# Kernel optimization log

Hardware: AMD Instinct MI355X
Metric: run time of the kernel (lower is better)

Reference implementation:

```python
import jax, jax.numpy as jnp
import numpy as np

H = 16  # num_heads

def setup_inputs() -> dict:
    key = jax.random.key(0)
    ks = jax.random.split(key, 5)
    d = 1024
    s = 0.02
    return {
        'x': jax.random.normal(ks[0], (2, 2048, d), jnp.float32),
        'Wq': jax.random.normal(ks[1], (d, d), jnp.float32) * s,
        'bq': jnp.zeros((d,), jnp.float32),
        'Wk': jax.random.normal(ks[2], (d, d), jnp.float32) * s,
        'bk': jnp.zeros((d,), jnp.float32),
        'Wv': jax.random.normal(ks[3], (d, d), jnp.float32) * s,
        'bv': jnp.zeros((d,), jnp.float32),
        'Wo': jax.random.normal(ks[4], (d, d), jnp.float32) * s,
        'bo': jnp.zeros((d,), jnp.float32),
        'ln_scale': jnp.ones((d,), jnp.float32),
        'ln_bias': jnp.zeros((d,), jnp.float32),
    }

def _layernorm(x, scale, bias, eps=1e-6):
    mu = jnp.mean(x, axis=-1, keepdims=True)
    var = jnp.var(x, axis=-1, keepdims=True)
    return (x - mu) * jax.lax.rsqrt(var + eps) * scale + bias

def reference(x, Wq, bq, Wk, bk, Wv, bv, Wo, bo, ln_scale, ln_bias):
    b, n, d = x.shape
    hd = d // H
    scale = hd ** -0.5
    residual = x
    xn = _layernorm(x, ln_scale, ln_bias)
    # QKV projections, split heads: [b, n, d] -> [b, H, n, hd]
    def split(y):
        return y.reshape(b, n, H, hd).transpose(0, 2, 1, 3)
    q = split(xn @ Wq + bq)
    k = split(xn @ Wk + bk)
    v = split(xn @ Wv + bv)
    attn = jnp.einsum('bhid,bhjd->bhij', q, k) * scale
    attn = jax.nn.softmax(attn, axis=-1)
    out = jnp.einsum('bhij,bhjd->bhid', attn, v)
    out = out.transpose(0, 2, 1, 3).reshape(b, n, d)
    out = out @ Wo + bo
    return out + residual
```

## Files before the change

### kernel.cpp

```cpp
#include <hip/hip_runtime.h>

typedef __bf16 bf16;
typedef __bf16 bf16x8 __attribute__((ext_vector_type(8)));
typedef float f32x4 __attribute__((ext_vector_type(4)));

#define D_MODEL 1024
#define SEQ 2048
#define NH 16
#define HD 64

#define GLD16(gp, lp) __builtin_amdgcn_global_load_lds( \
    (const __attribute__((address_space(1))) void*)(gp), \
    (__attribute__((address_space(3))) void*)(lp), 16, 0, 0)

__device__ __forceinline__ int sigi(int y) {
    return (y & 0x23) | ((y & 0x18) >> 1) | ((y & 0x04) << 2);
}

__global__ __launch_bounds__(256) void ln_kernel(const float* __restrict__ x,
        const float* __restrict__ g, const float* __restrict__ bta,
        bf16* __restrict__ xnb) {
    int tok = blockIdx.x;
    const float* xr = x + (size_t)tok * D_MODEL;
    float v[4];
    float s = 0.f, ss = 0.f;
#pragma unroll
    for (int j = 0; j < 4; ++j) {
        int idx = threadIdx.x + j * 256;
        float t = xr[idx];
        v[j] = t; s += t; ss += t * t;
    }
#pragma unroll
    for (int m = 32; m; m >>= 1) { s += __shfl_xor(s, m, 64); ss += __shfl_xor(ss, m, 64); }
    __shared__ float red_s[4], red_ss[4];
    int w = threadIdx.x >> 6;
    if ((threadIdx.x & 63) == 0) { red_s[w] = s; red_ss[w] = ss; }
    __syncthreads();
    s  = red_s[0] + red_s[1] + red_s[2] + red_s[3];
    ss = red_ss[0] + red_ss[1] + red_ss[2] + red_ss[3];
    float mu  = s * (1.f / D_MODEL);
    float var = ss * (1.f / D_MODEL) - mu * mu;
    float rstd = rsqrtf(var + 1e-6f);
    bf16* orow = xnb + (size_t)tok * D_MODEL;
#pragma unroll
    for (int j = 0; j < 4; ++j) {
        int idx = threadIdx.x + j * 256;
        float xn = (v[j] - mu) * rstd * g[idx] + bta[idx];
        orow[idx] = (bf16)xn;
    }
}

__global__ __launch_bounds__(256) void transpose_kernel(const float* __restrict__ W0,
        const float* __restrict__ W1, const float* __restrict__ W2,
        const float* __restrict__ W3, bf16* __restrict__ wt) {
    __shared__ float tile[32][33];
    int mat = blockIdx.z;
    const float* W = mat == 0 ? W0 : mat == 1 ? W1 : mat == 2 ? W2 : W3;
    bf16* dst = wt + (size_t)mat * D_MODEL * D_MODEL;
    int k0 = blockIdx.x * 32, n0 = blockIdx.y * 32;
    int tx = threadIdx.x & 31, ty0 = threadIdx.x >> 5;
#pragma unroll
    for (int r = 0; r < 4; ++r) {
        int ty = ty0 + r * 8;
        tile[ty][tx] = W[(size_t)(k0 + ty) * D_MODEL + n0 + tx];
    }
    __syncthreads();
#pragma unroll
    for (int r = 0; r < 4; ++r) {
        int ty = ty0 + r * 8;
        dst[(size_t)(n0 + ty) * D_MODEL + k0 + tx] = (bf16)tile[tx][ty];
    }
}

__global__ __launch_bounds__(256) void qkv_gemm(const bf16* __restrict__ A,
        const bf16* __restrict__ Bt, const float* __restrict__ bq,
        const float* __restrict__ bk, const float* __restrict__ bv,
        bf16* __restrict__ qo, bf16* __restrict__ ko, bf16* __restrict__ vto) {
    __shared__ __align__(16) bf16 As[128 * 32];
    __shared__ __align__(16) bf16 Bs[128 * 32];
    int m0 = blockIdx.x * 128, n0 = blockIdx.y * 128;
    int tid = threadIdx.x;
    int w = tid >> 6, l = tid & 63, lm = l & 15, lq = l >> 4;
    int wm = (w >> 1) * 64, wn = (w & 1) * 64;
    f32x4 acc[4][4] = {};
    const bf16* ag = A  + (size_t)(m0 + w * 32 + (l >> 2)) * D_MODEL + (l & 3) * 8;
    const bf16* bg = Bt + (size_t)(n0 + w * 32 + (l >> 2)) * D_MODEL + (l & 3) * 8;
    bf16* asd = &As[(w * 32) * 32];
    bf16* bsd = &Bs[(w * 32) * 32];
    for (int k0 = 0; k0 < D_MODEL; k0 += 32) {
        GLD16(ag,                asd);
        GLD16(ag + 16 * D_MODEL, asd + 16 * 32);
        GLD16(bg,                bsd);
        GLD16(bg + 16 * D_MODEL, bsd + 16 * 32);
        ag += 32; bg += 32;
        __syncthreads();
        bf16x8 af[4], bf_[4];
#pragma unroll
        for (int f = 0; f < 4; ++f) af[f]  = *(const bf16x8*)&As[(wm + f * 16 + lm) * 32 + lq * 8];
#pragma unroll
        for (int f = 0; f < 4; ++f) bf_[f] = *(const bf16x8*)&Bs[(wn + f * 16 + lm) * 32 + lq * 8];
#pragma unroll
        for (int fm = 0; fm < 4; ++fm)
#pragma unroll
            for (int fn = 0; fn < 4; ++fn)
                acc[fm][fn] = __builtin_amdgcn_mfma_f32_16x16x32_bf16(af[fm], bf_[fn], acc[fm][fn], 0, 0, 0);
        __syncthreads();
    }
#pragma unroll
    for (int fn = 0; fn < 4; ++fn) {
        int n_g = n0 + wn + fn * 16 + lm;
        int mat = n_g >> 10, within = n_g & 1023;
        int h = within >> 6, hdp = within & 63;
        float bias = mat == 0 ? bq[within] : mat == 1 ? bk[within] : bv[within];
#pragma unroll
        for (int fm = 0; fm < 4; ++fm) {
            int mg0 = m0 + wm + fm * 16 + lq * 4;
            int b_ = mg0 >> 11, i_base = mg0 & 2047;
            int bh = b_ * NH + h;
            if (mat == 0) {
#pragma unroll
                for (int r = 0; r < 4; ++r) {
                    float val = acc[fm][fn][r] + bias;
                    qo[((size_t)bh * SEQ + i_base + r) * HD + hdp] = (bf16)(val * 0.180336888f);
                }
            } else if (mat == 1) {
                int kc_ = hdp >> 5, lq_ = (hdp >> 3) & 3, e_ = hdp & 7;
#pragma unroll
                for (int r = 0; r < 4; ++r) {
                    int i = i_base + r;
                    int jt = i >> 6, jl = i & 63;
                    int idx = sigi(jl);
                    int nt_ = idx >> 4, lm_ = idx & 15;
                    ko[(size_t)bh * SEQ * HD + (size_t)jt * 4096 +
                       (kc_ * 4 + nt_) * 512 + (lq_ * 16 + lm_) * 8 + e_] =
                        (bf16)(acc[fm][fn][r] + bias);
                }
            } else {
                int nt_ = hdp >> 4, lm_ = hdp & 15;
                int jt = i_base >> 6, jl = i_base & 63;
                int kc_ = jl >> 5, lq_ = (jl >> 3) & 3, e0 = jl & 7;
                union { bf16 a[4]; uint2 u; } pk;
#pragma unroll
                for (int r = 0; r < 4; ++r) pk.a[r] = (bf16)(acc[fm][fn][r] + bias);
                *(uint2*)&vto[(size_t)bh * SEQ * HD + (size_t)jt * 4096 +
                              (kc_ * 4 + nt_) * 512 + (lq_ * 16 + lm_) * 8 + e0] = pk.u;
            }
        }
    }
}

__global__ __launch_bounds__(256) void attn_kernel(const bf16* __restrict__ q,
        const bf16* __restrict__ k, const bf16* __restrict__ vt,
        bf16* __restrict__ aout) {
    int bid = blockIdx.x;
    int xcd = bid & 7;
    int idx = bid >> 3;
    int bh  = xcd + 8 * (idx & 3);
    int i0  = (idx >> 2) * 128;
    int tid = threadIdx.x;
    int w = tid >> 6, l = tid & 63, lm = l & 15, lq = l >> 4;
    const bf16* qb = q  + (size_t)bh * SEQ * HD;
    const bf16* kp = k  + (size_t)bh * SEQ * HD + l * 8;
    const bf16* vp = vt + (size_t)bh * SEQ * HD + l * 8;

    bf16x8 qf[2][2];
#pragma unroll
    for (int mf = 0; mf < 2; ++mf)
#pragma unroll
        for (int kc = 0; kc < 2; ++kc)
            qf[mf][kc] = *(const bf16x8*)(qb + (size_t)(i0 + w * 32 + mf * 16 + lm) * HD + kc * 32 + lq * 8);

    bf16x8 kcur[2][4];
#pragma unroll
    for (int kc = 0; kc < 2; ++kc)
#pragma unroll
        for (int nt = 0; nt < 4; ++nt)
            kcur[kc][nt] = *(const bf16x8*)(kp + (kc * 4 + nt) * 512);
    kp += 4096;

    f32x4 o[2][4] = {};
    float l_acc[2] = {0.f, 0.f};

    for (int j0 = 0; j0 < SEQ; j0 += 64) {
        bf16x8 vcur[2][4];
#pragma unroll
        for (int kc = 0; kc < 2; ++kc)
#pragma unroll
            for (int nt = 0; nt < 4; ++nt)
                vcur[kc][nt] = *(const bf16x8*)(vp + (kc * 4 + nt) * 512);
        vp += 4096;
        bf16x8 knxt[2][4];
        if (j0 + 64 < SEQ) {
#pragma unroll
            for (int kc = 0; kc < 2; ++kc)
#pragma unroll
                for (int nt = 0; nt < 4; ++nt)
                    knxt[kc][nt] = *(const bf16x8*)(kp + (kc * 4 + nt) * 512);
            kp += 4096;
        }
        f32x4 s[2][4] = {};
#pragma unroll
        for (int kc = 0; kc < 2; ++kc)
#pragma unroll
            for (int nt = 0; nt < 4; ++nt) {
                s[0][nt] = __builtin_amdgcn_mfma_f32_16x16x32_bf16(kcur[kc][nt], qf[0][kc], s[0][nt], 0, 0, 0);
                s[1][nt] = __builtin_amdgcn_mfma_f32_16x16x32_bf16(kcur[kc][nt], qf[1][kc], s[1][nt], 0, 0, 0);
            }
#pragma unroll
        for (int mf = 0; mf < 2; ++mf) {
            float psum = 0.f;
#pragma unroll
            for (int nt = 0; nt < 4; ++nt)
#pragma unroll
                for (int r = 0; r < 4; ++r) {
                    float p = exp2f(s[mf][nt][r]);
                    s[mf][nt][r] = p; psum += p;
                }
            l_acc[mf] += psum;
        }
#pragma unroll
        for (int kc = 0; kc < 2; ++kc) {
            bf16x8 pf[2];
#pragma unroll
            for (int mf = 0; mf < 2; ++mf)
#pragma unroll
                for (int jj = 0; jj < 8; ++jj)
                    pf[mf][jj] = (bf16)s[mf][2 * kc + (jj >> 2)][jj & 3];
#pragma unroll
            for (int nt = 0; nt < 4; ++nt) {
                o[0][nt] = __builtin_amdgcn_mfma_f32_16x16x32_bf16(pf[0], vcur[kc][nt], o[0][nt], 0, 0, 0);
                o[1][nt] = __builtin_amdgcn_mfma_f32_16x16x32_bf16(pf[1], vcur[kc][nt], o[1][nt], 0, 0, 0);
            }
        }
#pragma unroll
        for (int kc = 0; kc < 2; ++kc)
#pragma unroll
            for (int nt = 0; nt < 4; ++nt)
                kcur[kc][nt] = knxt[kc][nt];
    }
    int b_ = bh >> 4, h = bh & 15;
#pragma unroll
    for (int mf = 0; mf < 2; ++mf) {
        l_acc[mf] += __shfl_xor(l_acc[mf], 16, 64);
        l_acc[mf] += __shfl_xor(l_acc[mf], 32, 64);
        float linv[4];
#pragma unroll
        for (int r = 0; r < 4; ++r)
            linv[r] = 1.f / __shfl(l_acc[mf], lq * 4 + r, 64);
#pragma unroll
        for (int nt = 0; nt < 4; ++nt) {
#pragma unroll
            for (int r = 0; r < 4; ++r) {
                int i = i0 + w * 32 + mf * 16 + lq * 4 + r;
                int tok = b_ * SEQ + i;
                aout[(size_t)tok * D_MODEL + h * HD + nt * 16 + lm] = (bf16)(o[mf][nt][r] * linv[r]);
            }
        }
    }
}

__global__ __launch_bounds__(256) void out_gemm(const bf16* __restrict__ A,
        const bf16* __restrict__ Bt, const float* __restrict__ bo,
        const float* __restrict__ resid, float* __restrict__ out) {
    __shared__ __align__(16) bf16 As[128 * 32];
    __shared__ __align__(16) bf16 Bs[128 * 32];
    int m0 = blockIdx.x * 128, n0 = blockIdx.y * 128;
    int tid = threadIdx.x;
    int w = tid >> 6, l = tid & 63, lm = l & 15, lq = l >> 4;
    int wm = (w >> 1) * 64, wn = (w & 1) * 64;
    f32x4 acc[4][4] = {};
    const bf16* ag = A  + (size_t)(m0 + w * 32 + (l >> 2)) * D_MODEL + (l & 3) * 8;
    const bf16* bg = Bt + (size_t)(n0 + w * 32 + (l >> 2)) * D_MODEL + (l & 3) * 8;
    bf16* asd = &As[(w * 32) * 32];
    bf16* bsd = &Bs[(w * 32) * 32];
    for (int k0 = 0; k0 < D_MODEL; k0 += 32) {
        GLD16(ag,                asd);
        GLD16(ag + 16 * D_MODEL, asd + 16 * 32);
        GLD16(bg,                bsd);
        GLD16(bg + 16 * D_MODEL, bsd + 16 * 32);
        ag += 32; bg += 32;
        __syncthreads();
        bf16x8 af[4], bf_[4];
#pragma unroll
        for (int f = 0; f < 4; ++f) af[f]  = *(const bf16x8*)&As[(wm + f * 16 + lm) * 32 + lq * 8];
#pragma unroll
        for (int f = 0; f < 4; ++f) bf_[f] = *(const bf16x8*)&Bs[(wn + f * 16 + lm) * 32 + lq * 8];
#pragma unroll
        for (int fm = 0; fm < 4; ++fm)
#pragma unroll
            for (int fn = 0; fn < 4; ++fn)
                acc[fm][fn] = __builtin_amdgcn_mfma_f32_16x16x32_bf16(af[fm], bf_[fn], acc[fm][fn], 0, 0, 0);
        __syncthreads();
    }
#pragma unroll
    for (int fn = 0; fn < 4; ++fn) {
        int n_g = n0 + wn + fn * 16 + lm;
        float bias = bo[n_g];
#pragma unroll
        for (int fm = 0; fm < 4; ++fm) {
#pragma unroll
            for (int r = 0; r < 4; ++r) {
                int m_g = m0 + wm + fm * 16 + lq * 4 + r;
                size_t idx = (size_t)m_g * D_MODEL + n_g;
                out[idx] = acc[fm][fn][r] + bias + resid[idx];
            }
        }
    }
}

extern "C" void kernel_launch(void* const* d_in, const int* in_sizes, int n_in,
                              void* d_out, int out_size, void* d_ws, size_t ws_size,
                              hipStream_t stream) {
    const float* x  = (const float*)d_in[0];
    const float* Wq = (const float*)d_in[1];
    const float* bq = (const float*)d_in[2];
    const float* Wk = (const float*)d_in[3];
    const float* bk = (const float*)d_in[4];
    const float* Wv = (const float*)d_in[5];
    const float* bv = (const float*)d_in[6];
    const float* Wo = (const float*)d_in[7];
    const float* bo = (const float*)d_in[8];
    const float* g  = (const float*)d_in[9];
    const float* bt = (const float*)d_in[10];
    (void)in_sizes; (void)n_in; (void)out_size; (void)ws_size;

    char* ws = (char*)d_ws;
    const size_t M8 = (size_t)8 << 20;
    bf16* xnb = (bf16*)(ws);
    bf16* wt  = (bf16*)(ws + M8);
    bf16* qb  = (bf16*)(ws + 2 * M8);
    bf16* kb  = (bf16*)(ws + 3 * M8);
    bf16* vtb = (bf16*)(ws + 4 * M8);
    bf16* ao  = xnb;
    float* out = (float*)d_out;

    ln_kernel<<<4096, 256, 0, stream>>>(x, g, bt, xnb);
    transpose_kernel<<<dim3(32, 32, 4), 256, 0, stream>>>(Wq, Wk, Wv, Wo, wt);
    qkv_gemm<<<dim3(32, 24), 256, 0, stream>>>(xnb, wt, bq, bk, bv, qb, kb, vtb);
    attn_kernel<<<512, 256, 0, stream>>>(qb, kb, vtb, ao);
    out_gemm<<<dim3(32, 8), 256, 0, stream>>>(ao, wt + (size_t)3 * D_MODEL * D_MODEL, bo, x, out);
}
```

Before: 217.9 us.

## Split attention over two key halves and merge partials in a combine kernel

The attention kernel now splits each query tile's key sequence into two halves, launching twice as many blocks. Each block writes unnormalized partial outputs and row sums to separate buffers. A new combine kernel adds the two partials and divides by the total row sum before the output projection. The aim is more parallelism and occupancy in attention, at the cost of an extra launch and extra global-memory traffic for the partials. The merge is a plain sum with no per-split max correction, so it is only valid because the softmax exponentials carry no max offset.

```diff
diff --git a/kernel.cpp b/kernel.cpp
--- a/kernel.cpp
+++ b/kernel.cpp
@@ -151,17 +151,21 @@
 
 __global__ __launch_bounds__(256) void attn_kernel(const bf16* __restrict__ q,
         const bf16* __restrict__ k, const bf16* __restrict__ vt,
-        bf16* __restrict__ aout) {
+        bf16* p0, bf16* p1, float* l0o, float* l1o) {
     int bid = blockIdx.x;
     int xcd = bid & 7;
-    int idx = bid >> 3;
-    int bh  = xcd + 8 * (idx & 3);
-    int i0  = (idx >> 2) * 128;
+    int t = bid >> 3;
+    int bh = xcd + 8 * (t & 3);
+    int t2 = t >> 2;
+    int i0 = (t2 >> 1) * 128;
+    int jh = t2 & 1;
+    bf16* po = jh ? p1 : p0;
+    float* lo = jh ? l1o : l0o;
     int tid = threadIdx.x;
     int w = tid >> 6, l = tid & 63, lm = l & 15, lq = l >> 4;
     const bf16* qb = q  + (size_t)bh * SEQ * HD;
-    const bf16* kp = k  + (size_t)bh * SEQ * HD + l * 8;
-    const bf16* vp = vt + (size_t)bh * SEQ * HD + l * 8;
+    const bf16* kp = k  + (size_t)bh * SEQ * HD + (size_t)jh * (SEQ / 2) * HD + l * 8;
+    const bf16* vp = vt + (size_t)bh * SEQ * HD + (size_t)jh * (SEQ / 2) * HD + l * 8;
 
     bf16x8 qf[2][2];
 #pragma unroll
@@ -181,7 +185,7 @@
     f32x4 o[2][4] = {};
     float l_acc[2] = {0.f, 0.f};
 
-    for (int j0 = 0; j0 < SEQ; j0 += 64) {
+    for (int j0 = 0; j0 < SEQ / 2; j0 += 64) {
         bf16x8 vcur[2][4];
 #pragma unroll
         for (int kc = 0; kc < 2; ++kc)
@@ -190,7 +194,7 @@
                 vcur[kc][nt] = *(const bf16x8*)(vp + (kc * 4 + nt) * 512);
         vp += 4096;
         bf16x8 knxt[2][4];
-        if (j0 + 64 < SEQ) {
+        if (j0 + 64 < SEQ / 2) {
 #pragma unroll
             for (int kc = 0; kc < 2; ++kc)
 #pragma unroll
@@ -243,20 +247,36 @@
     for (int mf = 0; mf < 2; ++mf) {
         l_acc[mf] += __shfl_xor(l_acc[mf], 16, 64);
         l_acc[mf] += __shfl_xor(l_acc[mf], 32, 64);
-        float linv[4];
-#pragma unroll
-        for (int r = 0; r < 4; ++r)
-            linv[r] = 1.f / __shfl(l_acc[mf], lq * 4 + r, 64);
+        if (lq == 0)
+            lo[(size_t)bh * SEQ + i0 + w * 32 + mf * 16 + lm] = l_acc[mf];
 #pragma unroll
         for (int nt = 0; nt < 4; ++nt) {
 #pragma unroll
             for (int r = 0; r < 4; ++r) {
                 int i = i0 + w * 32 + mf * 16 + lq * 4 + r;
                 int tok = b_ * SEQ + i;
-                aout[(size_t)tok * D_MODEL + h * HD + nt * 16 + lm] = (bf16)(o[mf][nt][r] * linv[r]);
-            }
-        }
-    }
+                po[(size_t)tok * D_MODEL + h * HD + nt * 16 + lm] = (bf16)o[mf][nt][r];
+            }
+        }
+    }
+}
+
+__global__ __launch_bounds__(256) void combine_kernel(const bf16* p0, const bf16* p1,
+        const float* __restrict__ l0, const float* __restrict__ l1, bf16* aout) {
+    int tok = blockIdx.x;
+    int b_ = tok >> 11, i = tok & 2047;
+    int col = threadIdx.x * 4;
+    int h = col >> 6;
+    size_t lidx = (size_t)(b_ * NH + h) * SEQ + i;
+    float inv = 1.f / (l0[lidx] + l1[lidx]);
+    union U { uint2 u; bf16 a[4]; } u0, u1, wr;
+    size_t base = (size_t)tok * D_MODEL + col;
+    u0.u = *(const uint2*)(p0 + base);
+    u1.u = *(const uint2*)(p1 + base);
+#pragma unroll
+    for (int e = 0; e < 4; ++e)
+        wr.a[e] = (bf16)(((float)u0.a[e] + (float)u1.a[e]) * inv);
+    *(uint2*)(aout + base) = wr.u;
 }
 
 __global__ __launch_bounds__(256) void out_gemm(const bf16* __restrict__ A,
@@ -331,12 +351,16 @@
     bf16* qb  = (bf16*)(ws + 2 * M8);
     bf16* kb  = (bf16*)(ws + 3 * M8);
     bf16* vtb = (bf16*)(ws + 4 * M8);
-    bf16* ao  = xnb;
+    bf16* p1  = (bf16*)(ws + 5 * M8);
+    float* l0 = (float*)(ws + 6 * M8);
+    float* l1 = l0 + (size_t)2 * NH * SEQ;
+    bf16* p0  = xnb;
     float* out = (float*)d_out;
 
     ln_kernel<<<4096, 256, 0, stream>>>(x, g, bt, xnb);
     transpose_kernel<<<dim3(32, 32, 4), 256, 0, stream>>>(Wq, Wk, Wv, Wo, wt);
     qkv_gemm<<<dim3(32, 24), 256, 0, stream>>>(xnb, wt, bq, bk, bv, qb, kb, vtb);
-    attn_kernel<<<512, 256, 0, stream>>>(qb, kb, vtb, ao);
-    out_gemm<<<dim3(32, 8), 256, 0, stream>>>(ao, wt + (size_t)3 * D_MODEL * D_MODEL, bo, x, out);
-}
+    attn_kernel<<<1024, 256, 0, stream>>>(qb, kb, vtb, p0, p1, l0, l1);
+    combine_kernel<<<4096, 256, 0, stream>>>(p0, p1, l0, l1, p0);
+    out_gemm<<<dim3(32, 8), 256, 0, stream>>>(p0, wt + (size_t)3 * D_MODEL * D_MODEL, bo, x, out);
+}
```

Result: faster. 211.3 us (-3.0%).
